# Optimization experiments

Measured on AMD Instinct MI355X. Metric: run time of the kernel, lower is better.

The kernel has to match this reference:

```python
import jax, jax.numpy as jnp
import numpy as np

NUM_CLASSES = 100
SLOTS_PER_CLASS = 1
NUM_SLOTS = NUM_CLASSES * SLOTS_PER_CLASS
DIM = 512
ITERS = 3
LOSS_STATUS = 1.0
POWER = 1


def setup_inputs() -> dict:
    key = jax.random.key(0)
    ks = jax.random.split(key, 10)
    b, n, d = 128, 1024, DIM
    s = 0.02
    return {
        "inputs": jax.random.normal(ks[0], (b, n, d), jnp.float32),
        "inputs_x": jax.random.normal(ks[1], (b, n, d), jnp.float32),
        "slots_mu": jax.random.normal(ks[2], (1, 1, d), jnp.float32),
        "slots_sigma": jax.random.normal(ks[3], (1, 1, d), jnp.float32),
        "to_q_w": jax.random.normal(ks[4], (d, d), jnp.float32) * s,
        "to_q_b": jnp.zeros((d,), jnp.float32),
        "to_k_w": jax.random.normal(ks[5], (d, d), jnp.float32) * s,
        "to_k_b": jnp.zeros((d,), jnp.float32),
        "w_ih": jax.random.normal(ks[6], (3 * d, d), jnp.float32) * s,
        "w_hh": jax.random.normal(ks[7], (3 * d, d), jnp.float32) * s,
        "b_ih": jnp.zeros((3 * d,), jnp.float32),
        "b_hh": jnp.zeros((3 * d,), jnp.float32),
    }


def _gru_cell(x, h, w_ih, w_hh, b_ih, b_hh):
    # x, h: [B, d]; PyTorch nn.GRU single-step equations
    gi = x @ w_ih.T + b_ih  # [B, 3d]
    gh = h @ w_hh.T + b_hh
    ir, iz, in_ = jnp.split(gi, 3, axis=-1)
    hr, hz, hn = jnp.split(gh, 3, axis=-1)
    r = jax.nn.sigmoid(ir + hr)
    z = jax.nn.sigmoid(iz + hz)
    nnew = jnp.tanh(in_ + r * hn)
    return (1.0 - z) * nnew + z * h


def reference(inputs, inputs_x, slots_mu, slots_sigma, to_q_w, to_q_b,
              to_k_w, to_k_b, w_ih, w_hh, b_ih, b_hh):
    b, n, d = inputs.shape
    scale = d ** (-0.5)
    # slots ~ Normal(mu, |sigma|) (reparameterized)
    noise = jax.random.normal(jax.random.key(1), (b, NUM_SLOTS, d), inputs.dtype)
    slots = slots_mu + jnp.abs(slots_sigma) * noise
    k = inputs @ to_k_w.T + to_k_b  # [b, n, d]
    attn = None
    updates = None
    for _ in range(ITERS):
        slots_prev = slots
        q = slots @ to_q_w.T + to_q_b  # [b, S, d]
        dots = jnp.einsum('bid,bjd->bij', q, k) * scale  # [b, S, n]
        attn = jax.nn.softmax(dots, axis=-1)
        updates = jnp.einsum('bjd,bij->bid', inputs_x, attn) / d  # [b, S, d]
        h = _gru_cell(updates.reshape(-1, d), slots_prev.reshape(-1, d),
                      w_ih, w_hh, b_ih, b_hh)
        slots = h.reshape(b, NUM_SLOTS, d)
    # slots_per_class == 1: no class aggregation needed
    slot_loss = jnp.sum(jax.nn.relu(attn)) / (b * NUM_SLOTS * n)
    out = LOSS_STATUS * jnp.sum(updates, axis=2)  # [b, NUM_SLOTS]
    return out, slot_loss ** POWER
```

## Files before the change

### kernel.cpp

```cpp
#include <hip/hip_runtime.h>
#include <math.h>

typedef __attribute__((ext_vector_type(4))) float f32x4;
typedef __attribute__((ext_vector_type(8))) short s16x8;

__device__ __forceinline__ unsigned rotl32(unsigned x, int r) {
    return (x << r) | (x >> (32 - r));
}
__device__ __forceinline__ unsigned short f2bf(float x) {
    unsigned u = __float_as_uint(x);
    unsigned r = (u + 0x7FFFu + ((u >> 16) & 1u)) >> 16;
    return (unsigned short)r;
}
__device__ __forceinline__ float b2f(unsigned short b) {
    return __uint_as_float((unsigned)b << 16);
}
__device__ __forceinline__ void async16(const unsigned short* g, unsigned short* l) {
    __builtin_amdgcn_global_load_lds(
        (const __attribute__((address_space(1))) void*)g,
        (__attribute__((address_space(3))) void*)l, 16, 0, 0);
}

__device__ __forceinline__ float bits_to_normal(unsigned bits) {
    float f = __uint_as_float((bits >> 9) | 0x3F800000u) - 1.0f;
    const float lo = -0.99999994f;
    float u = f * 2.0f + lo;
    u = fmaxf(lo, u);
    float w = -log1pf(-u * u);
    float p;
    if (w < 5.0f) {
        w -= 2.5f;
        p = 2.81022636e-08f;
        p = fmaf(p, w, 3.43273939e-07f);
        p = fmaf(p, w, -3.5233877e-06f);
        p = fmaf(p, w, -4.39150654e-06f);
        p = fmaf(p, w, 0.00021858087f);
        p = fmaf(p, w, -0.00125372503f);
        p = fmaf(p, w, -0.00417768164f);
        p = fmaf(p, w, 0.246640727f);
        p = fmaf(p, w, 1.50140941f);
    } else {
        w = sqrtf(w) - 3.0f;
        p = -0.000200214257f;
        p = fmaf(p, w, 0.000100950558f);
        p = fmaf(p, w, 0.00134934322f);
        p = fmaf(p, w, -0.00367342844f);
        p = fmaf(p, w, 0.00573950773f);
        p = fmaf(p, w, -0.0076224613f);
        p = fmaf(p, w, 0.00943887047f);
        p = fmaf(p, w, 1.00167406f);
        p = fmaf(p, w, 2.83297682f);
    }
    return 1.41421356237f * (p * u);
}

__global__ __launch_bounds__(256)
void k_init_slots(const float* __restrict__ mu, const float* __restrict__ sigma,
                  float* __restrict__ slots, unsigned short* __restrict__ slotsb) {
    unsigned e = blockIdx.x * 256u + threadIdx.x;
    const unsigned ks0 = 0u, ks1 = 1u, ks2 = 0x1BD11BDBu;
    unsigned x0 = 0u + ks0;
    unsigned x1 = e + ks1;
#define TF_RND(r) { x0 += x1; x1 = rotl32(x1, r); x1 ^= x0; }
    TF_RND(13) TF_RND(15) TF_RND(26) TF_RND(6)   x0 += ks1; x1 += ks2 + 1u;
    TF_RND(17) TF_RND(29) TF_RND(16) TF_RND(24)  x0 += ks2; x1 += ks0 + 2u;
    TF_RND(13) TF_RND(15) TF_RND(26) TF_RND(6)   x0 += ks0; x1 += ks1 + 3u;
    TF_RND(17) TF_RND(29) TF_RND(16) TF_RND(24)  x0 += ks1; x1 += ks2 + 4u;
    TF_RND(13) TF_RND(15) TF_RND(26) TF_RND(6)   x0 += ks2; x1 += ks0 + 5u;
#undef TF_RND
    unsigned bits = x0 ^ x1;
    int d0 = (int)(e & 511u);
    float v = mu[d0] + fabsf(sigma[d0]) * bits_to_normal(bits);
    slots[e] = v;
    slotsb[e] = f2bf(v);
}

__global__ __launch_bounds__(256)
void k_cast(const float* __restrict__ s, unsigned short* __restrict__ d, int n4) {
    int i = blockIdx.x * 256 + threadIdx.x;
    if (i < n4) {
        float4 v = ((const float4*)s)[i];
        ((ushort4*)d)[i] = make_ushort4(f2bf(v.x), f2bf(v.y), f2bf(v.z), f2bf(v.w));
    }
}

__global__ __launch_bounds__(256)
void k_transpose_cast(const float* __restrict__ x, unsigned short* __restrict__ xT) {
    __shared__ float t[32][33];
    int b = blockIdx.z;
    int j0 = blockIdx.x * 32;
    int d0 = blockIdx.y * 32;
    int tx = threadIdx.x & 31, ty = threadIdx.x >> 5;
    const float* xp = x + ((long long)b * 1024 + j0) * 512 + d0;
#pragma unroll
    for (int q = 0; q < 4; q++) {
        int j = ty + q * 8;
        t[j][tx] = xp[(long long)j * 512 + tx];
    }
    __syncthreads();
    unsigned short* op = xT + ((long long)b * 512 + d0) * 1024 + j0;
#pragma unroll
    for (int q = 0; q < 4; q++) {
        int d = ty + q * 8;
        op[(long long)d * 1024 + tx] = f2bf(t[tx][d]);
    }
}

template<bool A_F32, bool HAS_BIAS, bool XSWZ = false>
__global__ __launch_bounds__(256)
void k_mfma_nt(const void* __restrict__ Araw, long long sA,
               const unsigned short* __restrict__ B, long long sB,
               unsigned short* __restrict__ C, long long sC,
               const float* __restrict__ bias,
               int M, int N, int K, float alpha) {
    __shared__ __align__(16) unsigned short As[2][128 * 32];
    __shared__ __align__(16) unsigned short Bs[2][128 * 32];
    const int tid = threadIdx.x;
    const unsigned short* Ab = (const unsigned short*)Araw + (long long)blockIdx.z * sA;
    const float* Af = (const float*)Araw + (long long)blockIdx.z * sA;
    const unsigned short* Bb = B + (long long)blockIdx.z * sB;
    C += (long long)blockIdx.z * sC;

    int nb, mb;
    if (XSWZ) {
        unsigned L = blockIdx.x;
        unsigned x = L & 7u;
        unsigned j = L >> 3u;
        unsigned panels = gridDim.x >> 5u;
        mb = (int)(x * panels + (j >> 2u));
        nb = (int)(j & 3u);
    } else {
        nb = blockIdx.x;
        mb = blockIdx.y;
    }
    const int n0 = nb * 128;
    const int m0 = mb * 128;

    const int lane = tid & 63;
    const int wave = tid >> 6;
    const int wm = (wave >> 1) * 64;
    const int wn = (wave & 1) * 64;
    const int lrow = lane & 15;
    const int lquad = lane >> 4;

    f32x4 acc[4][4];
#pragma unroll
    for (int i = 0; i < 4; i++)
#pragma unroll
        for (int j = 0; j < 4; j++) acc[i][j] = (f32x4)0.0f;

    const int arow_s = tid >> 1;
    const int akh_s = (tid & 1) * 16;
    int arowg_s = m0 + arow_s; if (arowg_s >= M) arowg_s = M - 1;

    const int c0_row = tid >> 2;
    const int c0_kc = (tid & 3) * 8;
    const int ldsoff0 = (tid & ~63) * 8;
    const int ldsoff1 = (256 + (tid & ~63)) * 8;

    float4 f0, f1, f2, f3;

    auto loadAf32 = [&](int k0) {
        const float* ap = Af + (long long)arowg_s * K + k0 + akh_s;
        f0 = *(const float4*)(ap);
        f1 = *(const float4*)(ap + 4);
        f2 = *(const float4*)(ap + 8);
        f3 = *(const float4*)(ap + 12);
    };
    auto castA = [&](unsigned short* dst) {
        s16x8 p0, p1;
        p0[0] = (short)f2bf(f0.x); p0[1] = (short)f2bf(f0.y);
        p0[2] = (short)f2bf(f0.z); p0[3] = (short)f2bf(f0.w);
        p0[4] = (short)f2bf(f1.x); p0[5] = (short)f2bf(f1.y);
        p0[6] = (short)f2bf(f1.z); p0[7] = (short)f2bf(f1.w);
        p1[0] = (short)f2bf(f2.x); p1[1] = (short)f2bf(f2.y);
        p1[2] = (short)f2bf(f2.z); p1[3] = (short)f2bf(f2.w);
        p1[4] = (short)f2bf(f3.x); p1[5] = (short)f2bf(f3.y);
        p1[6] = (short)f2bf(f3.z); p1[7] = (short)f2bf(f3.w);
        *(s16x8*)&dst[arow_s * 32 + akh_s] = p0;
        *(s16x8*)&dst[arow_s * 32 + akh_s + 8] = p1;
    };
    auto stageAasync = [&](int k0, unsigned short* dst) {
        int r0 = m0 + c0_row;       if (r0 >= M) r0 = M - 1;
        int r1 = m0 + 64 + c0_row;  if (r1 >= M) r1 = M - 1;
        async16(Ab + (long long)r0 * K + k0 + c0_kc, &dst[ldsoff0]);
        async16(Ab + (long long)r1 * K + k0 + c0_kc, &dst[ldsoff1]);
    };
    auto stageB = [&](int k0, unsigned short* dst) {
        async16(Bb + (long long)(n0 + c0_row) * K + k0 + c0_kc, &dst[ldsoff0]);
        async16(Bb + (long long)(n0 + 64 + c0_row) * K + k0 + c0_kc, &dst[ldsoff1]);
    };

    const int nt = K >> 5;

    if (A_F32) {
        loadAf32(0);
        stageB(0, Bs[0]);
        castA(As[0]);
    } else {
        stageAasync(0, As[0]);
        stageB(0, Bs[0]);
    }
    __syncthreads();

    int cur = 0;
    for (int t = 0; t < nt; ++t) {
        const int nxt = cur ^ 1;
        const bool more = (t + 1 < nt);
        if (more) {
            const int k1 = (t + 1) << 5;
            if (A_F32) {
                loadAf32(k1);
            } else {
                stageAasync(k1, As[nxt]);
            }
            stageB(k1, Bs[nxt]);
        }
        const unsigned short* Asc = As[cur];
        const unsigned short* Bsc = Bs[cur];
        s16x8 afr[4], bfr[4];
#pragma unroll
        for (int i = 0; i < 4; i++)
            afr[i] = *(const s16x8*)&Asc[(wm + i * 16 + lrow) * 32 + lquad * 8];
#pragma unroll
        for (int j = 0; j < 4; j++)
            bfr[j] = *(const s16x8*)&Bsc[(wn + j * 16 + lrow) * 32 + lquad * 8];
#pragma unroll
        for (int i = 0; i < 4; i++)
#pragma unroll
            for (int j = 0; j < 4; j++)
                acc[i][j] = __builtin_amdgcn_mfma_f32_16x16x32_bf16(
                    afr[i], bfr[j], acc[i][j], 0, 0, 0);
        if (more && A_F32) castA(As[nxt]);
        __syncthreads();
        cur = nxt;
    }

#pragma unroll
    for (int i = 0; i < 4; i++) {
#pragma unroll
        for (int r = 0; r < 4; r++) {
            int grow = m0 + wm + i * 16 + lquad * 4 + r;
            if (grow < M) {
#pragma unroll
                for (int j = 0; j < 4; j++) {
                    int gcol = n0 + wn + j * 16 + lrow;
                    float v = acc[i][j][r] * alpha;
                    if (HAS_BIAS) v += bias[gcol];
                    C[(long long)grow * N + gcol] = f2bf(v);
                }
            }
        }
    }
}

__global__ __launch_bounds__(256)
void k_softmax_bf(unsigned short* __restrict__ attn) {
    __shared__ float red[8];
    unsigned short* p = attn + (long long)blockIdx.x * 1024;
    ushort4 v = ((const ushort4*)p)[threadIdx.x];
    float a0 = b2f(v.x), a1 = b2f(v.y), a2 = b2f(v.z), a3 = b2f(v.w);
    float mx = fmaxf(fmaxf(a0, a1), fmaxf(a2, a3));
#pragma unroll
    for (int off = 32; off; off >>= 1) mx = fmaxf(mx, __shfl_down(mx, off));
    int wid = threadIdx.x >> 6, lane = threadIdx.x & 63;
    if (lane == 0) red[wid] = mx;
    __syncthreads();
    mx = fmaxf(fmaxf(red[0], red[1]), fmaxf(red[2], red[3]));
    float e0 = expf(a0 - mx), e1 = expf(a1 - mx);
    float e2 = expf(a2 - mx), e3 = expf(a3 - mx);
    float s = (e0 + e1) + (e2 + e3);
#pragma unroll
    for (int off = 32; off; off >>= 1) s += __shfl_down(s, off);
    if (lane == 0) red[4 + wid] = s;
    __syncthreads();
    float inv = 1.0f / ((red[4] + red[5]) + (red[6] + red[7]));
    ((ushort4*)p)[threadIdx.x] =
        make_ushort4(f2bf(e0 * inv), f2bf(e1 * inv), f2bf(e2 * inv), f2bf(e3 * inv));
}

__global__ __launch_bounds__(256)
void k_gru_pw(const unsigned short* __restrict__ gi, const unsigned short* __restrict__ gh,
              const float* __restrict__ bih, const float* __restrict__ bhh,
              float* __restrict__ slots, unsigned short* __restrict__ slotsb) {
    long long idx = (long long)blockIdx.x * 256 + threadIdx.x;
    int m = (int)(idx >> 9);
    int c = (int)(idx & 511);
    const unsigned short* gim = gi + (long long)m * 1536;
    const unsigned short* ghm = gh + (long long)m * 1536;
    float r = 1.0f / (1.0f + expf(-(b2f(gim[c]) + b2f(ghm[c]) + bih[c] + bhh[c])));
    float z = 1.0f / (1.0f + expf(-(b2f(gim[512 + c]) + b2f(ghm[512 + c])
                                    + bih[512 + c] + bhh[512 + c])));
    float hn = b2f(ghm[1024 + c]) + bhh[1024 + c];
    float nn = tanhf(b2f(gim[1024 + c]) + bih[1024 + c] + r * hn);
    float hp = slots[idx];
    float h = (1.0f - z) * nn + z * hp;
    slots[idx] = h;
    slotsb[idx] = f2bf(h);
}

__global__ __launch_bounds__(128)
void k_out(const unsigned short* __restrict__ updb, float* __restrict__ out) {
    __shared__ float r2[2];
    const unsigned short* p = updb + (long long)blockIdx.x * 512;
    ushort4 v = ((const ushort4*)p)[threadIdx.x];
    float s = (b2f(v.x) + b2f(v.y)) + (b2f(v.z) + b2f(v.w));
#pragma unroll
    for (int off = 32; off; off >>= 1) s += __shfl_down(s, off);
    if ((threadIdx.x & 63) == 0) r2[threadIdx.x >> 6] = s;
    __syncthreads();
    if (threadIdx.x == 0) {
        out[blockIdx.x] = r2[0] + r2[1];
        if (blockIdx.x == 0) out[12800] = 0.0009765625f;
    }
}

extern "C" void kernel_launch(void* const* d_in, const int* in_sizes, int n_in,
                              void* d_out, int out_size, void* d_ws, size_t ws_size,
                              hipStream_t stream) {
    const float* inputs   = (const float*)d_in[0];
    const float* inputs_x = (const float*)d_in[1];
    const float* mu       = (const float*)d_in[2];
    const float* sigma    = (const float*)d_in[3];
    const float* to_q_w   = (const float*)d_in[4];
    const float* to_q_b   = (const float*)d_in[5];
    const float* to_k_w   = (const float*)d_in[6];
    const float* to_k_b   = (const float*)d_in[7];
    const float* w_ih     = (const float*)d_in[8];
    const float* w_hh     = (const float*)d_in[9];
    const float* b_ih     = (const float*)d_in[10];
    const float* b_hh     = (const float*)d_in[11];
    float* out = (float*)d_out;

    char* base = (char*)d_ws;
    unsigned short* k_bf   = (unsigned short*)(base);
    unsigned short* xT     = (unsigned short*)(base + 134217728ll);
    float*          slots  = (float*)        (base + 268435456ll);
    unsigned short* slotsb = (unsigned short*)(base + 294649856ll);
    unsigned short* updb   = (unsigned short*)(base + 307757056ll);
    char* regionA          = base + 320864256ll;
    char* regionB          = base + 360185856ll;
    unsigned short* Wk_bf  = (unsigned short*)(base + 399507456ll);
    unsigned short* Wq_bf  = (unsigned short*)(base + 400031744ll);
    unsigned short* Wih_bf = (unsigned short*)(base + 400556032ll);
    unsigned short* Whh_bf = (unsigned short*)(base + 402128896ll);
    unsigned short* q_bf   = (unsigned short*)regionA;
    unsigned short* gi_bf  = (unsigned short*)regionA;
    unsigned short* attnb  = (unsigned short*)regionB;
    unsigned short* gh_bf  = (unsigned short*)regionB;

    k_init_slots<<<25600, 256, 0, stream>>>(mu, sigma, slots, slotsb);
    k_cast<<<256, 256, 0, stream>>>(to_k_w, Wk_bf, 65536);
    k_cast<<<256, 256, 0, stream>>>(to_q_w, Wq_bf, 65536);
    k_cast<<<768, 256, 0, stream>>>(w_ih, Wih_bf, 196608);
    k_cast<<<768, 256, 0, stream>>>(w_hh, Whh_bf, 196608);
    k_transpose_cast<<<dim3(32, 16, 128), 256, 0, stream>>>(inputs_x, xT);

    k_mfma_nt<true, true, true><<<dim3(4096, 1, 1), 256, 0, stream>>>(
        inputs, 0, Wk_bf, 0, k_bf, 0, to_k_b, 131072, 512, 512, 1.0f);

    const float scale = 0.044194173824159216f;
    for (int it = 0; it < 3; ++it) {
        k_mfma_nt<false, true><<<dim3(4, 100, 1), 256, 0, stream>>>(
            slotsb, 0, Wq_bf, 0, q_bf, 0, to_q_b, 12800, 512, 512, 1.0f);
        k_mfma_nt<false, false><<<dim3(8, 1, 128), 256, 0, stream>>>(
            q_bf, 51200, k_bf, 524288, attnb, 102400, nullptr, 100, 1024, 512, scale);
        k_softmax_bf<<<12800, 256, 0, stream>>>(attnb);
        k_mfma_nt<false, false><<<dim3(4, 1, 128), 256, 0, stream>>>(
            attnb, 102400, xT, 524288, updb, 51200, nullptr, 100, 512, 1024, 0.001953125f);
        k_mfma_nt<false, false><<<dim3(12, 100, 1), 256, 0, stream>>>(
            updb, 0, Wih_bf, 0, gi_bf, 0, nullptr, 12800, 1536, 512, 1.0f);
        k_mfma_nt<false, false><<<dim3(12, 100, 1), 256, 0, stream>>>(
            slotsb, 0, Whh_bf, 0, gh_bf, 0, nullptr, 12800, 1536, 512, 1.0f);
        k_gru_pw<<<25600, 256, 0, stream>>>(gi_bf, gh_bf, b_ih, b_hh, slots, slotsb);
    }
    k_out<<<12800, 128, 0, stream>>>(updb, out);
}
```

Before: 1.448 ms.

## Fold key projection into query side to skip the large K GEMM

Uses the identity q·k = (q Wk)·x + q·bk to precompute G = Wq^T Wk style combined weight and a folded bias, so attention dots are computed directly against a bf16 cast of the inputs instead of first projecting all 131072 tokens through Wk. This removes the large [131072x512x512] K-projection GEMM, replacing it with a plain cast of inputs and a tiny 512x512 weight product. The key bias term is dropped as constant per row under softmax. It adds extra rounding from bf16 fused weights.

```diff
diff --git a/kernel.cpp b/kernel.cpp
--- a/kernel.cpp
+++ b/kernel.cpp
@@ -104,6 +104,34 @@
         int d = ty + q * 8;
         op[(long long)d * 1024 + tx] = f2bf(t[tx][d]);
     }
+}
+
+__global__ __launch_bounds__(256)
+void k_transpose_cast_512(const float* __restrict__ W, unsigned short* __restrict__ WT) {
+    __shared__ float t[32][33];
+    int r0 = blockIdx.y * 32;
+    int c0 = blockIdx.x * 32;
+    int tx = threadIdx.x & 31, ty = threadIdx.x >> 5;
+#pragma unroll
+    for (int q = 0; q < 4; q++) {
+        int i = ty + q * 8;
+        t[i][tx] = W[(r0 + i) * 512 + c0 + tx];
+    }
+    __syncthreads();
+#pragma unroll
+    for (int q = 0; q < 4; q++) {
+        int i = ty + q * 8;
+        WT[(c0 + i) * 512 + r0 + tx] = f2bf(t[tx][i]);
+    }
+}
+
+__global__ __launch_bounds__(64)
+void k_bias_fold(const float* __restrict__ bq, const float* __restrict__ Wk,
+                 float* __restrict__ c) {
+    int d = blockIdx.x * 64 + threadIdx.x;
+    float s = 0.0f;
+    for (int e = 0; e < 512; e++) s += bq[e] * Wk[e * 512 + d];
+    c[d] = s;
 }
 
 template<bool A_F32, bool HAS_BIAS, bool XSWZ = false>
@@ -333,38 +361,41 @@
     float* out = (float*)d_out;
 
     char* base = (char*)d_ws;
-    unsigned short* k_bf   = (unsigned short*)(base);
+    unsigned short* inp_bf = (unsigned short*)(base);
     unsigned short* xT     = (unsigned short*)(base + 134217728ll);
     float*          slots  = (float*)        (base + 268435456ll);
     unsigned short* slotsb = (unsigned short*)(base + 294649856ll);
     unsigned short* updb   = (unsigned short*)(base + 307757056ll);
     char* regionA          = base + 320864256ll;
     char* regionB          = base + 360185856ll;
-    unsigned short* Wk_bf  = (unsigned short*)(base + 399507456ll);
-    unsigned short* Wq_bf  = (unsigned short*)(base + 400031744ll);
+    unsigned short* WkT_bf = (unsigned short*)(base + 399507456ll);
+    unsigned short* WqT_bf = (unsigned short*)(base + 400031744ll);
     unsigned short* Wih_bf = (unsigned short*)(base + 400556032ll);
     unsigned short* Whh_bf = (unsigned short*)(base + 402128896ll);
-    unsigned short* q_bf   = (unsigned short*)regionA;
+    unsigned short* Gt_bf  = (unsigned short*)(base + 403701760ll);
+    float*          c_fold = (float*)        (base + 404226048ll);
+    unsigned short* qk_bf  = (unsigned short*)regionA;
     unsigned short* gi_bf  = (unsigned short*)regionA;
     unsigned short* attnb  = (unsigned short*)regionB;
     unsigned short* gh_bf  = (unsigned short*)regionB;
 
     k_init_slots<<<25600, 256, 0, stream>>>(mu, sigma, slots, slotsb);
-    k_cast<<<256, 256, 0, stream>>>(to_k_w, Wk_bf, 65536);
-    k_cast<<<256, 256, 0, stream>>>(to_q_w, Wq_bf, 65536);
     k_cast<<<768, 256, 0, stream>>>(w_ih, Wih_bf, 196608);
     k_cast<<<768, 256, 0, stream>>>(w_hh, Whh_bf, 196608);
+    k_cast<<<65536, 256, 0, stream>>>(inputs, inp_bf, 16777216);
     k_transpose_cast<<<dim3(32, 16, 128), 256, 0, stream>>>(inputs_x, xT);
-
-    k_mfma_nt<true, true, true><<<dim3(4096, 1, 1), 256, 0, stream>>>(
-        inputs, 0, Wk_bf, 0, k_bf, 0, to_k_b, 131072, 512, 512, 1.0f);
+    k_transpose_cast_512<<<dim3(16, 16), 256, 0, stream>>>(to_k_w, WkT_bf);
+    k_transpose_cast_512<<<dim3(16, 16), 256, 0, stream>>>(to_q_w, WqT_bf);
+    k_bias_fold<<<8, 64, 0, stream>>>(to_q_b, to_k_w, c_fold);
+    k_mfma_nt<false, false><<<dim3(4, 4, 1), 256, 0, stream>>>(
+        WkT_bf, 0, WqT_bf, 0, Gt_bf, 0, nullptr, 512, 512, 512, 1.0f);
 
     const float scale = 0.044194173824159216f;
     for (int it = 0; it < 3; ++it) {
         k_mfma_nt<false, true><<<dim3(4, 100, 1), 256, 0, stream>>>(
-            slotsb, 0, Wq_bf, 0, q_bf, 0, to_q_b, 12800, 512, 512, 1.0f);
+            slotsb, 0, Gt_bf, 0, qk_bf, 0, c_fold, 12800, 512, 512, 1.0f);
         k_mfma_nt<false, false><<<dim3(8, 1, 128), 256, 0, stream>>>(
-            q_bf, 51200, k_bf, 524288, attnb, 102400, nullptr, 100, 1024, 512, scale);
+            qk_bf, 51200, inp_bf, 524288, attnb, 102400, nullptr, 100, 1024, 512, scale);
         k_softmax_bf<<<12800, 256, 0, stream>>>(attnb);
         k_mfma_nt<false, false><<<dim3(4, 1, 128), 256, 0, stream>>>(
             attnb, 102400, xT, 524288, updb, 51200, nullptr, 100, 512, 1024, 0.001953125f);
```

Result: faster. 1.357 ms (-6.3%).
